# Kernel optimization log

Hardware: AMD Instinct MI355X
Metric: run time of the kernel (lower is better)

## Reference

```python
import jax, jax.numpy as jnp
import numpy as np

HEIGHT, WIDTH = 480, 640
IN_CHANNEL, OUT_CHANNEL, FILTER = 6, 32, 3
B, N = 8, 16384
X_COL, Y_COL, P_COL = 1, 2, 3


def setup_inputs() -> dict:
    key = jax.random.key(0)
    k1, k2, k3, k4 = jax.random.split(key, 4)
    xytp = jax.random.uniform(k1, (B, N, 4), dtype=jnp.float32)
    features = jax.random.normal(k2, (B, N, IN_CHANNEL), dtype=jnp.float32)
    fan_in = FILTER * FILTER * (IN_CHANNEL + 2)
    W = jax.random.normal(k3, (FILTER, FILTER, IN_CHANNEL + 2, OUT_CHANNEL), dtype=jnp.float32) / jnp.sqrt(jnp.float32(fan_in))
    bias = jax.random.normal(k4, (OUT_CHANNEL,), dtype=jnp.float32) * 0.05
    return {"xytp": xytp, "features": features, "W": W, "bias": bias}


def reference(xytp, features, W, bias):
    Bc, Nc = xytp.shape[:2]
    # polarity channels: [pos, neg] concatenated with extra features -> Cin = in_channel + 2
    p = xytp[..., P_COL:P_COL + 1]
    feat = jnp.concatenate([p, 1.0 - p, features], axis=-1)  # [B, N, Cin]
    # event2image: round normalized coords to integer pixel grid (values in [0, H] / [0, W])
    yy = jnp.round(xytp[..., Y_COL] * HEIGHT).astype(jnp.int32)  # [B, N]
    xx = jnp.round(xytp[..., X_COL] * WIDTH).astype(jnp.int32)   # [B, N]
    H1, W1 = HEIGHT + 1, WIDTH + 1
    Cin = feat.shape[-1]
    bidx = jnp.broadcast_to(jnp.arange(Bc)[:, None], (Bc, Nc))
    # scn.InputLayer(mode=3): sum features at duplicate coordinates -> dense scatter-add
    grid = jnp.zeros((Bc, H1, W1, Cin), feat.dtype).at[bidx, yy, xx].add(feat)
    # SubmanifoldConvolution: inactive sites hold zero features, so a dense SAME conv
    # computes the identical gather+GEMM+scatter result at every active site.
    out_grid = jax.lax.conv_general_dilated(
        grid, W, window_strides=(1, 1), padding='SAME',
        dimension_numbers=('NHWC', 'HWIO', 'NHWC')) + bias
    # scn.OutputLayer: each input event reads the feature at its (b, y, x) site
    return out_grid[bidx, yy, xx]  # [B, N, out_channel]
```

## Files before the change

### kernel.cpp

```cpp
#include <hip/hip_runtime.h>
#include <hip/hip_bf16.h>

#define HEIGHT 480
#define WIDTH  640
#define IN_CH  6
#define CIN    8
#define COUT   32
#define BATCH  8
#define NPTS   16384
#define NPTOT  (BATCH * NPTS)
#define GH 483
#define GW 643
#define NCELLS ((size_t)BATCH * GH * GW)
#define NW64   38824
#define SENTINEL 0xFFFFFFFFu

typedef float f32x2 __attribute__((ext_vector_type(2)));

__device__ __forceinline__ size_t cell_idx(int b, int gy, int gx) {
    return ((size_t)b * GH + gy) * GW + gx;
}

__device__ __forceinline__ void point_cell(const float4 q, int point,
                                           int& b, int& gy, int& gx) {
    gy = (int)rintf(q.z * (float)HEIGHT) + 1;
    gx = (int)rintf(q.y * (float)WIDTH) + 1;
    b  = point >> 14;
}

__global__ void zero_masks_kernel(uint4* __restrict__ m4, int n4) {
    int i = blockIdx.x * blockDim.x + threadIdx.x;
    if (i < n4) m4[i] = make_uint4(0u, 0u, 0u, 0u);
}

__global__ void scatter_kernel(const float4* __restrict__ xytp,
                               const float*  __restrict__ feats,
                               unsigned long long* __restrict__ occ,
                               unsigned int* __restrict__ over_idx,
                               float4* __restrict__ over_val,
                               float* __restrict__ grid) {
    int point = blockIdx.x * blockDim.x + threadIdx.x;
    if (point >= NPTOT) return;
    float4 q = xytp[point];
    int b, gy, gx;
    point_cell(q, point, b, gy, gx);
    size_t ci = cell_idx(b, gy, gx);

    const float* f = feats + (size_t)point * IN_CH;
    float v0 = q.w, v1 = 1.0f - q.w;
    float f0 = f[0], f1 = f[1], f2 = f[2], f3 = f[3], f4 = f[4], f5 = f[5];

    unsigned long long bit = 1ull << (ci & 63);
    unsigned long long old = atomicOr(&occ[ci >> 6], bit);
    bool collider = (old & bit) != 0ull;

    over_idx[point] = collider ? (unsigned int)ci : SENTINEL;

    if (!collider) {
        float* cell = grid + (ci << 3);
        *(float4*)(cell)     = make_float4(v0, v1, f0, f1);
        *(float4*)(cell + 4) = make_float4(f2, f3, f4, f5);
    } else {
        over_val[2 * point]     = make_float4(v0, v1, f0, f1);
        over_val[2 * point + 1] = make_float4(f2, f3, f4, f5);
    }
}

__global__ void fix_kernel(const unsigned int* __restrict__ over_idx,
                           const float4* __restrict__ over_val,
                           float* __restrict__ grid) {
    int point = blockIdx.x * blockDim.x + threadIdx.x;
    if (point >= NPTOT) return;
    unsigned int ci32 = over_idx[point];
    if (ci32 == SENTINEL) return;
    size_t ci = ci32;
    float4 a = over_val[2 * point];
    float4 d = over_val[2 * point + 1];
    float* cell = grid + (ci << 3);
    unsafeAtomicAdd(cell + 0, a.x);
    unsafeAtomicAdd(cell + 1, a.y);
    unsafeAtomicAdd(cell + 2, a.z);
    unsafeAtomicAdd(cell + 3, a.w);
    unsafeAtomicAdd(cell + 4, d.x);
    unsafeAtomicAdd(cell + 5, d.y);
    unsafeAtomicAdd(cell + 6, d.z);
    unsafeAtomicAdd(cell + 7, d.w);
}

__global__ void __launch_bounds__(256)
conv_gather_kernel(const float4* __restrict__ xytp,
                   const float*  __restrict__ grid,
                   const unsigned long long* __restrict__ occ,
                   const float*  __restrict__ W,
                   const float*  __restrict__ bias,
                   float* __restrict__ out) {
    int point = blockIdx.x * blockDim.x + threadIdx.x;
    if (point >= NPTOT) return;
    float4 q = xytp[point];
    int b, gy, gx;
    point_cell(q, point, b, gy, gx);
    size_t center  = cell_idx(b, gy, gx);
    size_t base_ci = center - GW - 1;

    unsigned int occ9 = 0;
#pragma unroll
    for (int ky = 0; ky < 3; ++ky) {
        size_t ci_row = base_ci + (size_t)ky * GW;
        size_t w  = ci_row >> 6;
        int    sh = (int)(ci_row & 63);
        unsigned long long v = occ[w] >> sh;
        if (sh >= 62) v |= occ[w + 1] << (64 - sh);
        occ9 |= ((unsigned int)v & 7u) << (ky * 3);
    }

    float4 g0[9], g1[9];
#pragma unroll
    for (int k = 0; k < 9; ++k) {
        if (occ9 & (1u << k)) {
            size_t ci = base_ci + (size_t)(k / 3) * GW + (k % 3);
            const float* cell = grid + (ci << 3);
            g0[k] = *(const float4*)(cell);
            g1[k] = *(const float4*)(cell + 4);
        }
    }

    const f32x2* bias2 = (const f32x2*)bias;
    f32x2 acc[16];
#pragma unroll
    for (int c = 0; c < 16; ++c) acc[c] = bias2[c];

#pragma unroll
    for (int k = 0; k < 9; ++k) {
        if (occ9 & (1u << k)) {
            float4 a = g0[k], d = g1[k];
            float gv[CIN] = {a.x, a.y, a.z, a.w, d.x, d.y, d.z, d.w};
            const float* wp = W + k * CIN * COUT;
#pragma unroll
            for (int ci2 = 0; ci2 < CIN; ++ci2) {
                const f32x2* w2 = (const f32x2*)(wp + ci2 * COUT);
                f32x2 gg = {gv[ci2], gv[ci2]};
#pragma unroll
                for (int c = 0; c < 16; ++c) {
                    acc[c] = __builtin_elementwise_fma(gg, w2[c], acc[c]);
                }
            }
        }
    }

    float* o = out + (size_t)point * COUT;
#pragma unroll
    for (int c = 0; c < 8; ++c) {
        *(float4*)(o + c * 4) = make_float4(acc[2 * c].x, acc[2 * c].y,
                                            acc[2 * c + 1].x, acc[2 * c + 1].y);
    }
}

extern "C" void kernel_launch(void* const* d_in, const int* in_sizes, int n_in,
                              void* d_out, int out_size, void* d_ws, size_t ws_size,
                              hipStream_t stream) {
    const float4* xytp  = (const float4*)d_in[0];
    const float*  feats = (const float*)d_in[1];
    const float*  W     = (const float*)d_in[2];
    const float*  bias  = (const float*)d_in[3];
    float* out = (float*)d_out;

    float* grid = (float*)d_ws;
    const size_t grid_bytes = NCELLS * CIN * sizeof(float);
    char* p = (char*)d_ws + grid_bytes;
    unsigned long long* occ      = (unsigned long long*)p;
    unsigned int*       over_idx = (unsigned int*)(p + (size_t)NW64 * 8);
    float4*             over_val = (float4*)(p + (size_t)NW64 * 8 + (size_t)NPTOT * 4);
    (void)ws_size;

    const int blk = 256;
    const int nblk_pts = (NPTOT + blk - 1) / blk;

    const int n4 = (int)(((size_t)NW64 * 8) / 16);
    zero_masks_kernel<<<(n4 + blk - 1) / blk, blk, 0, stream>>>((uint4*)occ, n4);

    scatter_kernel<<<nblk_pts, blk, 0, stream>>>(xytp, feats, occ,
                                                 over_idx, over_val, grid);

    fix_kernel<<<nblk_pts, blk, 0, stream>>>(over_idx, over_val, grid);

    conv_gather_kernel<<<nblk_pts, blk, 0, stream>>>(xytp, grid, occ, W, bias, out);
}
```

Before: 39.58 us.

## Split conv gather across two lanes per point with shuffle reduction

The conv gather kernel now uses two threads per event point. Each thread handles the even or odd taps of the 3x3 window and part of the occupancy-mask reads, then the partial accumulators are combined with cross-lane shuffles, and each lane writes half of the 32 outputs. This doubles thread-level parallelism and splits the memory latency of the neighbour gathers, at the cost of double the coordinate and xytp work per point, shuffle overhead, and uneven tap counts (5 versus 4) between the two lanes.

```diff
diff --git a/kernel.cpp b/kernel.cpp
--- a/kernel.cpp
+++ b/kernel.cpp
@@ -26,6 +26,12 @@
     gy = (int)rintf(q.z * (float)HEIGHT) + 1;
     gx = (int)rintf(q.y * (float)WIDTH) + 1;
     b  = point >> 14;
+}
+
+__device__ __forceinline__ unsigned int row_bits(unsigned long long a,
+                                                 unsigned long long a2, int sh) {
+    unsigned long long v = sh ? ((a >> sh) | (a2 << (64 - sh))) : a;
+    return (unsigned int)v & 7u;
 }
 
 __global__ void zero_masks_kernel(uint4* __restrict__ m4, int n4) {
@@ -94,64 +100,85 @@
                    const float*  __restrict__ W,
                    const float*  __restrict__ bias,
                    float* __restrict__ out) {
-    int point = blockIdx.x * blockDim.x + threadIdx.x;
-    if (point >= NPTOT) return;
+    int tid = blockIdx.x * blockDim.x + threadIdx.x;
+    int point = tid >> 1;
+    int sub   = tid & 1;
+
     float4 q = xytp[point];
     int b, gy, gx;
     point_cell(q, point, b, gy, gx);
     size_t center  = cell_idx(b, gy, gx);
     size_t base_ci = center - GW - 1;
 
-    unsigned int occ9 = 0;
-#pragma unroll
-    for (int ky = 0; ky < 3; ++ky) {
-        size_t ci_row = base_ci + (size_t)ky * GW;
-        size_t w  = ci_row >> 6;
-        int    sh = (int)(ci_row & 63);
-        unsigned long long v = occ[w] >> sh;
-        if (sh >= 62) v |= occ[w + 1] << (64 - sh);
-        occ9 |= ((unsigned int)v & 7u) << (ky * 3);
-    }
-
-    float4 g0[9], g1[9];
+    size_t cr0 = base_ci + (size_t)(sub ? 2 : 0) * GW;
+    size_t w0 = cr0 >> 6;  int sh0 = (int)(cr0 & 63);
+    unsigned long long A  = occ[w0];
+    unsigned long long A2 = occ[w0 + 1];
+    size_t cr1 = base_ci + (size_t)GW;
+    size_t w1 = cr1 >> 6;  int sh1 = (int)(cr1 & 63);
+    unsigned long long B = 0, B2 = 0;
+    if (!sub) { B = occ[w1]; B2 = occ[w1 + 1]; }
+
+    unsigned int mybits;
+    if (!sub) mybits = row_bits(A, A2, sh0) | (row_bits(B, B2, sh1) << 3);
+    else      mybits = row_bits(A, A2, sh0) << 6;
+    unsigned int occ9 = mybits | (unsigned int)__shfl_xor((int)mybits, 1);
+
+    float4 g0[5], g1[5];
 #pragma unroll
     for (int k = 0; k < 9; ++k) {
-        if (occ9 & (1u << k)) {
-            size_t ci = base_ci + (size_t)(k / 3) * GW + (k % 3);
-            const float* cell = grid + (ci << 3);
-            g0[k] = *(const float4*)(cell);
-            g1[k] = *(const float4*)(cell + 4);
+        if ((k & 1) == sub) {
+            if (occ9 & (1u << k)) {
+                size_t ci = base_ci + (size_t)(k / 3) * GW + (k % 3);
+                const float* cell = grid + (ci << 3);
+                g0[k >> 1] = *(const float4*)(cell);
+                g1[k >> 1] = *(const float4*)(cell + 4);
+            }
         }
     }
 
     const f32x2* bias2 = (const f32x2*)bias;
     f32x2 acc[16];
 #pragma unroll
-    for (int c = 0; c < 16; ++c) acc[c] = bias2[c];
+    for (int c = 0; c < 16; ++c) {
+        f32x2 z = {0.0f, 0.0f};
+        acc[c] = sub ? z : bias2[c];
+    }
 
 #pragma unroll
     for (int k = 0; k < 9; ++k) {
-        if (occ9 & (1u << k)) {
-            float4 a = g0[k], d = g1[k];
-            float gv[CIN] = {a.x, a.y, a.z, a.w, d.x, d.y, d.z, d.w};
-            const float* wp = W + k * CIN * COUT;
-#pragma unroll
-            for (int ci2 = 0; ci2 < CIN; ++ci2) {
-                const f32x2* w2 = (const f32x2*)(wp + ci2 * COUT);
-                f32x2 gg = {gv[ci2], gv[ci2]};
-#pragma unroll
-                for (int c = 0; c < 16; ++c) {
-                    acc[c] = __builtin_elementwise_fma(gg, w2[c], acc[c]);
+        if ((k & 1) == sub) {
+            if (occ9 & (1u << k)) {
+                float4 a = g0[k >> 1], d = g1[k >> 1];
+                float gv[CIN] = {a.x, a.y, a.z, a.w, d.x, d.y, d.z, d.w};
+                const float* wp = W + k * CIN * COUT;
+#pragma unroll
+                for (int ci2 = 0; ci2 < CIN; ++ci2) {
+                    const f32x2* w2 = (const f32x2*)(wp + ci2 * COUT);
+                    f32x2 gg = {gv[ci2], gv[ci2]};
+#pragma unroll
+                    for (int c = 0; c < 16; ++c) {
+                        acc[c] = __builtin_elementwise_fma(gg, w2[c], acc[c]);
+                    }
                 }
             }
         }
     }
 
-    float* o = out + (size_t)point * COUT;
+    f32x2 res[8];
 #pragma unroll
     for (int c = 0; c < 8; ++c) {
-        *(float4*)(o + c * 4) = make_float4(acc[2 * c].x, acc[2 * c].y,
-                                            acc[2 * c + 1].x, acc[2 * c + 1].y);
+        f32x2 mine  = sub ? acc[8 + c] : acc[c];
+        f32x2 other = sub ? acc[c]     : acc[8 + c];
+        res[c].x = mine.x + __shfl_xor(other.x, 1);
+        res[c].y = mine.y + __shfl_xor(other.y, 1);
+    }
+
+    float* o = out + (size_t)point * COUT + sub * 16;
+#pragma unroll
+    for (int c = 0; c < 4; ++c) {
+        *(float4*)(o + c * 4) = make_float4(res[2 * c].x, res[2 * c].y,
+                                            res[2 * c + 1].x, res[2 * c + 1].y);
     }
 }
 
@@ -183,5 +210,6 @@
 
     fix_kernel<<<nblk_pts, blk, 0, stream>>>(over_idx, over_val, grid);
 
-    conv_gather_kernel<<<nblk_pts, blk, 0, stream>>>(xytp, grid, occ, W, bias, out);
-}
+    conv_gather_kernel<<<(NPTOT * 2) / blk, blk, 0, stream>>>(xytp, grid, occ,
+                                                              W, bias, out);
+}
```

Measured after the change: 42.62 us. 1.08x slower.
